# Kernel tuning notes

Measured on AMD Instinct MI355X. Metric: run time of the kernel, lower is better.

## Reference

```python
import jax, jax.numpy as jnp
import numpy as np

D_MODEL = 768
N_HEADS = 12
D_FF = 3072
B, T = 1, 4096
EPS = 1e-5


def _linear_params(key, d_in, d_out):
    kw, kb = jax.random.split(key)
    s = 1.0 / np.sqrt(d_in)
    W = jax.random.uniform(kw, (d_in, d_out), jnp.float32, -s, s)
    b = jax.random.uniform(kb, (d_out,), jnp.float32, -s, s)
    return W, b


def setup_inputs() -> dict:
    key = jax.random.key(0)
    keys = jax.random.split(key, 8)
    x = jax.random.normal(keys[0], (B, T, D_MODEL), jnp.float32)
    Wq, bq = _linear_params(keys[1], D_MODEL, D_MODEL)
    Wk, bk = _linear_params(keys[2], D_MODEL, D_MODEL)
    Wv, bv = _linear_params(keys[3], D_MODEL, D_MODEL)
    Wo, bo = _linear_params(keys[4], D_MODEL, D_MODEL)
    W1, b1 = _linear_params(keys[5], D_MODEL, D_FF)
    W2, b2 = _linear_params(keys[6], D_FF, D_MODEL)
    g1 = jnp.ones((D_MODEL,), jnp.float32)
    be1 = jnp.zeros((D_MODEL,), jnp.float32)
    g2 = jnp.ones((D_MODEL,), jnp.float32)
    be2 = jnp.zeros((D_MODEL,), jnp.float32)
    return {"x": x, "Wq": Wq, "bq": bq, "Wk": Wk, "bk": bk, "Wv": Wv, "bv": bv,
            "Wo": Wo, "bo": bo, "W1": W1, "b1": b1, "W2": W2, "b2": b2,
            "g1": g1, "be1": be1, "g2": g2, "be2": be2}


def _layer_norm(x, g, b):
    mu = jnp.mean(x, axis=-1, keepdims=True)
    var = jnp.var(x, axis=-1, keepdims=True)
    return (x - mu) * jax.lax.rsqrt(var + EPS) * g + b


def reference(x, Wq, bq, Wk, bk, Wv, bv, Wo, bo, W1, b1, W2, b2, g1, be1, g2, be2):
    b_, t_, d_ = x.shape
    dk = d_ // N_HEADS
    # QKV projections -> [B, H, T, dk]
    def split_heads(y):
        return y.reshape(b_, t_, N_HEADS, dk).transpose(0, 2, 1, 3)
    q = split_heads(x @ Wq + bq)
    k = split_heads(x @ Wk + bk)
    v = split_heads(x @ Wv + bv)
    # scores [B, H, T, T], causal mask, softmax
    scores = jnp.einsum('bhqd,bhkd->bhqk', q, k) / np.sqrt(dk).astype(np.float32)
    causal = jnp.tril(jnp.ones((t_, t_), dtype=bool))
    scores = jnp.where(causal, scores, -jnp.inf)
    attn = jax.nn.softmax(scores, axis=-1)
    out = jnp.einsum('bhqk,bhkd->bhqd', attn, v)
    out = out.transpose(0, 2, 1, 3).reshape(b_, t_, d_)
    attn_out = out @ Wo + bo
    # residual + LN1
    h = _layer_norm(x + attn_out, g1, be1)
    # FFN
    ff = jax.nn.relu(h @ W1 + b1) @ W2 + b2
    # residual + LN2
    return _layer_norm(h + ff, g2, be2)
```

## Files before the change

kernel.cpp:

```cpp
#include <hip/hip_runtime.h>
#include <math.h>

#define TSEQ 4096
#define DMODEL 768
#define NHEADS 12
#define DKH 64
#define DFF 3072
#define LOG2E 1.44269504f

typedef __attribute__((ext_vector_type(4))) float f32x4;
typedef __attribute__((ext_vector_type(8))) short s16x8;
typedef unsigned short u16;
typedef unsigned int u32;

__device__ __forceinline__ u16 f2bf(float x) {
    u32 u = __builtin_bit_cast(u32, x);
    u32 r = u + 0x7FFFu + ((u >> 16) & 1u);
    return (u16)(r >> 16);
}
__device__ __forceinline__ float bf2f(u16 h) {
    u32 u = ((u32)h) << 16;
    return __builtin_bit_cast(float, u);
}
__device__ __forceinline__ u32 cvtpk(float lo, float hi) {
    u32 r;
    asm("v_cvt_pk_bf16_f32 %0, %1, %2" : "=v"(r) : "v"(lo), "v"(hi));
    return r;
}

__device__ __forceinline__ void gll16(const void* g, void* lds) {
    __builtin_amdgcn_global_load_lds(
        (const __attribute__((address_space(1))) u32*)g,
        (__attribute__((address_space(3))) u32*)lds, 16, 0, 0);
}

__global__ __launch_bounds__(256) void tobf16(const float* __restrict__ in,
                                              u16* __restrict__ out, int n4)
{
    int idx = blockIdx.x * 256 + threadIdx.x;
    for (int i = idx; i < n4; i += 262144) {
        float4 v = *(const float4*)(in + (size_t)i * 4);
        *(ushort4*)(out + (size_t)i * 4) =
            make_ushort4(f2bf(v.x), f2bf(v.y), f2bf(v.z), f2bf(v.w));
    }
}

__global__ __launch_bounds__(256) void wtrans4(
    const float* __restrict__ Wq, const float* __restrict__ Wk,
    const float* __restrict__ Wv, const float* __restrict__ Wo,
    u16* __restrict__ Wqkvt, u16* __restrict__ Wot)
{
    __shared__ float t[32 * 33];
    const int z = blockIdx.z;
    const float* W = (z == 0) ? Wq : (z == 1) ? Wk : (z == 2) ? Wv : Wo;
    u16* out = (z < 3) ? Wqkvt : Wot;
    const int nofs = (z < 3) ? z * 768 : 0;
    const int K = 768, N = 768;
    const int tid = threadIdx.x;
    const int kt = blockIdx.y << 5, nt = blockIdx.x << 5;
    const int r = tid >> 3, c4 = tid & 7;
    float4 v = *(const float4*)(W + (size_t)(kt + r) * N + nt + (c4 << 2));
    t[r * 33 + (c4 << 2) + 0] = v.x;
    t[r * 33 + (c4 << 2) + 1] = v.y;
    t[r * 33 + (c4 << 2) + 2] = v.z;
    t[r * 33 + (c4 << 2) + 3] = v.w;
    __syncthreads();
    float a0 = t[((c4 << 2) + 0) * 33 + r];
    float a1 = t[((c4 << 2) + 1) * 33 + r];
    float a2 = t[((c4 << 2) + 2) * 33 + r];
    float a3 = t[((c4 << 2) + 3) * 33 + r];
    u16* o = out + (size_t)(nofs + nt + r) * K + kt + (c4 << 2);
    *(ushort4*)o = make_ushort4(f2bf(a0), f2bf(a1), f2bf(a2), f2bf(a3));
}

__global__ __launch_bounds__(256) void wtrans(const float* __restrict__ W,
                                              u16* __restrict__ out,
                                              int K, int N)
{
    __shared__ float t[32 * 33];
    const int tid = threadIdx.x;
    const int kt = blockIdx.y << 5, nt = blockIdx.x << 5;
    const int r = tid >> 3, c4 = tid & 7;
    float4 v = *(const float4*)(W + (size_t)(kt + r) * N + nt + (c4 << 2));
    t[r * 33 + (c4 << 2) + 0] = v.x;
    t[r * 33 + (c4 << 2) + 1] = v.y;
    t[r * 33 + (c4 << 2) + 2] = v.z;
    t[r * 33 + (c4 << 2) + 3] = v.w;
    __syncthreads();
    float a0 = t[((c4 << 2) + 0) * 33 + r];
    float a1 = t[((c4 << 2) + 1) * 33 + r];
    float a2 = t[((c4 << 2) + 2) * 33 + r];
    float a3 = t[((c4 << 2) + 3) * 33 + r];
    u16* o = out + (size_t)(nt + r) * K + kt + (c4 << 2);
    *(ushort4*)o = make_ushort4(f2bf(a0), f2bf(a1), f2bf(a2), f2bf(a3));
}

__global__ __launch_bounds__(256) void bias_cat_kernel(const float* bq, const float* bk,
                                                       const float* bv, float* o)
{
    int i = blockIdx.x * 256 + threadIdx.x;
    if (i < 768) o[i] = bq[i];
    else if (i < 1536) o[i] = bk[i - 768];
    else if (i < 2304) o[i] = bv[i - 1536];
}

template<int BM, int BN, int EPI>
__global__ __launch_bounds__(256) void gemm_bf(
    const u16* __restrict__ A, const u16* __restrict__ B,
    const float* __restrict__ bias, const float* __restrict__ R,
    float* __restrict__ Cf, u16* __restrict__ Cs,
    u16* __restrict__ Qb, u16* __restrict__ Kb, u16* __restrict__ VTb,
    int N, int KP)
{
    constexpr int FM = BM / 32, FN = BN / 32, NC = BN / 2, NCP = NC + 4;
    __shared__ u16 As[BM * 64];
    __shared__ u16 Bs[BN * 64];
    __shared__ float Ep[4 * 16 * NCP];

    const int tid = threadIdx.x;
    const int w = tid >> 6, lane = tid & 63;
    const int wr = w >> 1, wc = w & 1;
    const int li = lane & 15, g = lane >> 4;

    const int gX = gridDim.x;
    const int nwg = gridDim.x * gridDim.y;
    const int wid = blockIdx.y * gX + blockIdx.x;
    const int qc = nwg >> 3;
    const int nid = (wid & 7) * qc + (wid >> 3);
    const int m0 = (nid / gX) * BM, n0 = (nid % gX) * BN;

    f32x4 acc[FM][FN];
#pragma unroll
    for (int mi = 0; mi < FM; ++mi)
#pragma unroll
        for (int ni = 0; ni < FN; ++ni) acc[mi][ni] = (f32x4){0.f, 0.f, 0.f, 0.f};

    const int row8 = lane >> 3;
    const int cs = (lane & 7) ^ row8;
    const int l7 = li & 7;

    for (int k0 = 0; k0 < KP; k0 += 64) {
        __syncthreads();
#pragma unroll
        for (int i = 0; i < BM / 32; ++i) {
            int inst = w * (BM / 32) + i;
            const u16* gp = A + (size_t)(m0 + inst * 8 + row8) * KP + k0 + cs * 8;
            gll16(gp, &As[inst * 512]);
        }
#pragma unroll
        for (int i = 0; i < BN / 32; ++i) {
            int inst = w * (BN / 32) + i;
            const u16* gp = B + (size_t)(n0 + inst * 8 + row8) * KP + k0 + cs * 8;
            gll16(gp, &Bs[inst * 512]);
        }
        __syncthreads();
        s16x8 af[FM][2], bfr[FN][2];
#pragma unroll
        for (int mi = 0; mi < FM; ++mi) {
            int Ra = wr * (BM / 2) + mi * 16 + li;
#pragma unroll
            for (int dc = 0; dc < 2; ++dc)
                af[mi][dc] = *(const s16x8*)&As[Ra * 64 + ((dc * 4 + g) ^ l7) * 8];
        }
#pragma unroll
        for (int ni = 0; ni < FN; ++ni) {
            int Rb = wc * (BN / 2) + ni * 16 + li;
#pragma unroll
            for (int dc = 0; dc < 2; ++dc)
                bfr[ni][dc] = *(const s16x8*)&Bs[Rb * 64 + ((dc * 4 + g) ^ l7) * 8];
        }
        __builtin_amdgcn_s_setprio(1);
#pragma unroll
        for (int mi = 0; mi < FM; ++mi)
#pragma unroll
            for (int ni = 0; ni < FN; ++ni) {
                acc[mi][ni] = __builtin_amdgcn_mfma_f32_16x16x32_bf16(
                    af[mi][0], bfr[ni][0], acc[mi][ni], 0, 0, 0);
                acc[mi][ni] = __builtin_amdgcn_mfma_f32_16x16x32_bf16(
                    af[mi][1], bfr[ni][1], acc[mi][ni], 0, 0, 0);
            }
        __builtin_amdgcn_s_setprio(0);
    }
    __syncthreads();

    float* ep = Ep + w * 16 * NCP;
    const int colbase = n0 + wc * NC;
    const int rr = lane >> 2, ch = lane & 3;

#pragma unroll
    for (int mi = 0; mi < FM; ++mi) {
#pragma unroll
        for (int ni = 0; ni < FN; ++ni)
#pragma unroll
            for (int r = 0; r < 4; ++r)
                ep[(g * 4 + r) * NCP + ni * 16 + li] = acc[mi][ni][r];
        asm volatile("s_waitcnt lgkmcnt(0)" ::: "memory");

        const int grow0 = m0 + wr * (BM / 2) + mi * 16;
        const int grow = grow0 + rr;

        if constexpr (EPI == 1) {
#pragma unroll
            for (int q = 0; q < NC / 16; ++q) {
                int col = ch * (NC / 4) + q * 4;
                f32x4 v = *(f32x4*)&ep[rr * NCP + col];
                int gn = colbase + col;
                float4 bb = *(const float4*)(bias + gn);
                float4 rv = *(const float4*)(R + (size_t)grow * N + gn);
                float4 ov;
                ov.x = v[0] + bb.x + rv.x; ov.y = v[1] + bb.y + rv.y;
                ov.z = v[2] + bb.z + rv.z; ov.w = v[3] + bb.w + rv.w;
                *(float4*)(Cf + (size_t)grow * N + gn) = ov;
            }
        } else if constexpr (EPI == 2) {
#pragma unroll
            for (int q = 0; q < NC / 16; ++q) {
                int col = ch * (NC / 4) + q * 4;
                f32x4 v = *(f32x4*)&ep[rr * NCP + col];
                int gn = colbase + col;
                float4 bb = *(const float4*)(bias + gn);
                float x0 = fmaxf(v[0] + bb.x, 0.f), x1 = fmaxf(v[1] + bb.y, 0.f);
                float x2 = fmaxf(v[2] + bb.z, 0.f), x3 = fmaxf(v[3] + bb.w, 0.f);
                *(ushort4*)(Cs + (size_t)grow * N + gn) =
                    make_ushort4(f2bf(x0), f2bf(x1), f2bf(x2), f2bf(x3));
            }
        } else {
            const int seg = colbase / 768;
            const int hh = (colbase % 768) >> 6;
            if (seg < 2) {
                u16* dst = (seg == 0) ? Qb : Kb;
                const float sc2 = (seg == 0) ? 0.125f * LOG2E : 1.0f;
#pragma unroll
                for (int q = 0; q < NC / 16; ++q) {
                    int col = ch * (NC / 4) + q * 4;
                    f32x4 v = *(f32x4*)&ep[rr * NCP + col];
                    float4 bb = *(const float4*)(bias + colbase + col);
                    u16 h0 = f2bf((v[0] + bb.x) * sc2);
                    u16 h1 = f2bf((v[1] + bb.y) * sc2);
                    u16 h2 = f2bf((v[2] + bb.z) * sc2);
                    u16 h3 = f2bf((v[3] + bb.w) * sc2);
                    *(ushort4*)&dst[((size_t)(hh << 12) + grow) * 64 + col] =
                        make_ushort4(h0, h1, h2, h3);
                }
            } else {
                float bb = bias[colbase + lane];
                s16x8 pa, pb;
#pragma unroll
                for (int r2 = 0; r2 < 8; ++r2)
                    pa[r2] = (short)f2bf(ep[r2 * NCP + lane] + bb);
#pragma unroll
                for (int r2 = 0; r2 < 8; ++r2)
                    pb[r2] = (short)f2bf(ep[(8 + r2) * NCP + lane] + bb);
                u16* ov = VTb + ((size_t)(hh << 6) + lane) * TSEQ + grow0;
                *(s16x8*)(ov)     = pa;
                *(s16x8*)(ov + 8) = pb;
            }
        }
    }
}

__global__ __launch_bounds__(256) void attn64(
    const u16* __restrict__ Qb, const u16* __restrict__ Kb,
    const u16* __restrict__ VTb, u16* __restrict__ ctxb)
{
    __shared__ u16 Ks[2][4096];
    __shared__ u16 Vs[2][4096];
    __shared__ u16 Ps[4][1024];

    const int tid = threadIdx.x, w = tid >> 6, lane = tid & 63;
    const int g = lane >> 4, li = lane & 15, l7 = lane & 7;
    const int wid = blockIdx.x;
    const int nid = (wid & 7) * 48 + (wid >> 3);
    const int h = nid >> 5;
    const int p = nid & 31;

    const u16* Qh = Qb + ((size_t)h << 18);
    const u16* Kh = Kb + ((size_t)h << 18);
    const u16* Vh = VTb + ((size_t)h << 18);

    const int row8 = lane >> 3;
    const int cs = (lane & 7) ^ row8;

    for (int pass = 0; pass < 2; ++pass) {
        const int qbk = pass ? 63 - p : p;
        const int q0 = qbk << 6;
        const int nkb = qbk + 1;

        s16x8 qf[2];
#pragma unroll
        for (int dc = 0; dc < 2; ++dc)
            qf[dc] = *(const s16x8*)(Qh + (size_t)(q0 + w * 16 + li) * 64 + dc * 32 + g * 8);

        const u16* kbase = Kh + (size_t)(w * 16 + row8) * 64 + cs * 8;
        const u16* vbase = Vh + (size_t)(w * 16 + row8) * TSEQ + cs * 8;

        f32x4 o[4];
        float m_ = -1e30f, l_ = 0.f;
#pragma unroll
        for (int d16 = 0; d16 < 4; ++d16) o[d16] = (f32x4){0.f, 0.f, 0.f, 0.f};

#pragma unroll
        for (int i = 0; i < 2; ++i) {
            int inst = w * 2 + i;
            gll16(kbase + (size_t)i * 512, &Ks[0][inst * 512]);
            gll16(vbase + (size_t)i * 8 * TSEQ, &Vs[0][inst * 512]);
        }
        __syncthreads();

        for (int kb = 0; kb < nkb; ++kb) {
            const int cur = kb & 1;
            if (kb + 1 < nkb) {
                const int kn = kb + 1;
#pragma unroll
                for (int i = 0; i < 2; ++i) {
                    int inst = w * 2 + i;
                    gll16(kbase + (size_t)kn * 4096 + (size_t)i * 512, &Ks[cur ^ 1][inst * 512]);
                    gll16(vbase + (size_t)kn * 64 + (size_t)i * 8 * TSEQ, &Vs[cur ^ 1][inst * 512]);
                }
            }

            f32x4 s[4];
            __builtin_amdgcn_s_setprio(1);
#pragma unroll
            for (int c = 0; c < 4; ++c) {
                s[c] = (f32x4){0.f, 0.f, 0.f, 0.f};
                s16x8 a0 = *(const s16x8*)&Ks[cur][(c * 16 + li) * 64 + ((g) ^ l7) * 8];
                s16x8 a1 = *(const s16x8*)&Ks[cur][(c * 16 + li) * 64 + ((4 + g) ^ l7) * 8];
                s[c] = __builtin_amdgcn_mfma_f32_16x16x32_bf16(a0, qf[0], s[c], 0, 0, 0);
                s[c] = __builtin_amdgcn_mfma_f32_16x16x32_bf16(a1, qf[1], s[c], 0, 0, 0);
            }
            __builtin_amdgcn_s_setprio(0);

            if (kb == qbk) {
#pragma unroll
                for (int c = 0; c < 4; ++c)
#pragma unroll
                    for (int r = 0; r < 4; ++r) {
                        int kglob = (kb << 6) + c * 16 + g * 4 + r;
                        int qglob = q0 + w * 16 + li;
                        if (kglob > qglob) s[c][r] = -1e30f;
                    }
            }

            float v0 = fmaxf(fmaxf(s[0][0], s[0][1]), fmaxf(s[0][2], s[0][3]));
            float v1 = fmaxf(fmaxf(s[1][0], s[1][1]), fmaxf(s[1][2], s[1][3]));
            float v2 = fmaxf(fmaxf(s[2][0], s[2][1]), fmaxf(s[2][2], s[2][3]));
            float v3 = fmaxf(fmaxf(s[3][0], s[3][1]), fmaxf(s[3][2], s[3][3]));
            float pmp = fmaxf(fmaxf(v0, v1), fmaxf(v2, v3));

            if (!__all(pmp <= m_ + 8.f)) {
                float pm = fmaxf(pmp, __shfl_xor(pmp, 16, 64));
                pm = fmaxf(pm, __shfl_xor(pm, 32, 64));
                float mn = fmaxf(m_, pm);
                float sc2 = exp2f(m_ - mn);
                m_ = mn;
                l_ *= sc2;
#pragma unroll
                for (int r = 0; r < 4; ++r) {
                    float os = __shfl(sc2, g * 4 + r, 64);
#pragma unroll
                    for (int d16 = 0; d16 < 4; ++d16) o[d16][r] *= os;
                }
            }

#pragma unroll
            for (int c = 0; c < 4; ++c) {
                float e0 = exp2f(s[c][0] - m_);
                float e1 = exp2f(s[c][1] - m_);
                float e2 = exp2f(s[c][2] - m_);
                float e3 = exp2f(s[c][3] - m_);
                l_ += (e0 + e1) + (e2 + e3);
                u32 r0 = cvtpk(e0, e1);
                u32 r1 = cvtpk(e2, e3);
                *(uint2*)&Ps[w][li * 64 + ((c * 16 + 4 * g) ^ (l7 << 3))] =
                    make_uint2(r0, r1);
            }

            asm volatile("s_waitcnt lgkmcnt(0)" ::: "memory");
            __builtin_amdgcn_sched_barrier(0);

            __builtin_amdgcn_s_setprio(1);
#pragma unroll
            for (int ks = 0; ks < 2; ++ks) {
                int koff = ((ks * 4 + g) ^ l7) * 8;
                s16x8 pf = *(const s16x8*)&Ps[w][li * 64 + ((ks * 32 + g * 8) ^ (l7 << 3))];
#pragma unroll
                for (int d16 = 0; d16 < 4; ++d16) {
                    s16x8 vf = *(const s16x8*)&Vs[cur][(d16 * 16 + li) * 64 + koff];
                    o[d16] = __builtin_amdgcn_mfma_f32_16x16x32_bf16(pf, vf, o[d16], 0, 0, 0);
                }
            }
            __builtin_amdgcn_s_setprio(0);
            __syncthreads();
        }

        l_ += __shfl_xor(l_, 16, 64);
        l_ += __shfl_xor(l_, 32, 64);
        float il = 1.0f / l_;
#pragma unroll
        for (int r = 0; r < 4; ++r) {
            float iv = __shfl(il, g * 4 + r, 64);
            int qrow = q0 + w * 16 + g * 4 + r;
#pragma unroll
            for (int d16 = 0; d16 < 4; ++d16) {
                int col = (h << 6) + d16 * 16 + li;
                ctxb[(size_t)qrow * DMODEL + col] = f2bf(o[d16][r] * iv);
            }
        }
        __syncthreads();
    }
}

template<int BF>
__global__ __launch_bounds__(256) void ln_kernel(const float* __restrict__ in,
    const float* __restrict__ gw, const float* __restrict__ bw,
    float* __restrict__ outf, u16* __restrict__ outb)
{
    __shared__ float red[8];
    const int row = blockIdx.x, tid = threadIdx.x;
    const float* x = in + (size_t)row * DMODEL;
    float v0 = x[tid], v1 = x[tid + 256], v2 = x[tid + 512];
    float s = v0 + v1 + v2;
#pragma unroll
    for (int off = 32; off > 0; off >>= 1) s += __shfl_xor(s, off, 64);
    const int wv = tid >> 6, lane = tid & 63;
    if (lane == 0) red[wv] = s;
    __syncthreads();
    float mu = (red[0] + red[1] + red[2] + red[3]) * (1.0f / DMODEL);
    float d0 = v0 - mu, d1 = v1 - mu, d2 = v2 - mu;
    float s2 = d0 * d0 + d1 * d1 + d2 * d2;
#pragma unroll
    for (int off = 32; off > 0; off >>= 1) s2 += __shfl_xor(s2, off, 64);
    if (lane == 0) red[4 + wv] = s2;
    __syncthreads();
    float var = (red[4] + red[5] + red[6] + red[7]) * (1.0f / DMODEL);
    float rstd = rsqrtf(var + 1e-5f);
    float y0 = d0 * rstd * gw[tid] + bw[tid];
    float y1 = d1 * rstd * gw[tid + 256] + bw[tid + 256];
    float y2 = d2 * rstd * gw[tid + 512] + bw[tid + 512];
    float* yo = outf + (size_t)row * DMODEL;
    yo[tid] = y0; yo[tid + 256] = y1; yo[tid + 512] = y2;
    if constexpr (BF) {
        u16* o = outb + (size_t)row * DMODEL;
        o[tid] = f2bf(y0); o[tid + 256] = f2bf(y1); o[tid + 512] = f2bf(y2);
    }
}

extern "C" void kernel_launch(void* const* d_in, const int* in_sizes, int n_in,
                              void* d_out, int out_size, void* d_ws, size_t ws_size,
                              hipStream_t stream)
{
    const float* x  = (const float*)d_in[0];
    const float* Wq = (const float*)d_in[1];  const float* bq = (const float*)d_in[2];
    const float* Wk = (const float*)d_in[3];  const float* bk = (const float*)d_in[4];
    const float* Wv = (const float*)d_in[5];  const float* bv = (const float*)d_in[6];
    const float* Wo = (const float*)d_in[7];  const float* bo = (const float*)d_in[8];
    const float* W1 = (const float*)d_in[9];  const float* b1 = (const float*)d_in[10];
    const float* W2 = (const float*)d_in[11]; const float* b2 = (const float*)d_in[12];
    const float* g1 = (const float*)d_in[13]; const float* be1 = (const float*)d_in[14];
    const float* g2 = (const float*)d_in[15]; const float* be2 = (const float*)d_in[16];
    float* out = (float*)d_out;

    char* wsb = (char*)d_ws;
    u16*   xb    = (u16*)(wsb + 0);
    u16*   Wqkvt = (u16*)(wsb + 6291456);
    u16*   Wot   = (u16*)(wsb + 9830400);
    u16*   W1t   = (u16*)(wsb + 11010048);
    u16*   W2t   = (u16*)(wsb + 15728640);
    float* bcat  = (float*)(wsb + 20447232);
    u16*   Qb    = (u16*)(wsb + 20456448);
    u16*   Kb2   = (u16*)(wsb + 26747904);
    u16*   VTb   = (u16*)(wsb + 33039360);
    u16*   ctxb  = (u16*)(wsb + 39330816);
    float* s1    = (float*)(wsb + 45622272);
    float* h     = (float*)(wsb + 58205184);
    u16*   hb    = (u16*)(wsb + 70788096);
    u16*   ff1b  = (u16*)(wsb + 77079552);
    float* t2    = (float*)(wsb + 102245376);

    tobf16<<<1024, 256, 0, stream>>>(x, xb, 786432);
    wtrans4<<<dim3(24, 24, 4), 256, 0, stream>>>(Wq, Wk, Wv, Wo, Wqkvt, Wot);
    wtrans<<<dim3(96, 24), 256, 0, stream>>>(W1, W1t, 768, 3072);
    wtrans<<<dim3(24, 96), 256, 0, stream>>>(W2, W2t, 3072, 768);
    bias_cat_kernel<<<9, 256, 0, stream>>>(bq, bk, bv, bcat);

    gemm_bf<128, 128, 0><<<dim3(18, 32), 256, 0, stream>>>(
        xb, Wqkvt, bcat, nullptr, nullptr, nullptr, Qb, Kb2, VTb, 2304, 768);
    attn64<<<384, 256, 0, stream>>>(Qb, Kb2, VTb, ctxb);
    gemm_bf<64, 128, 1><<<dim3(6, 64), 256, 0, stream>>>(
        ctxb, Wot, bo, x, s1, nullptr, nullptr, nullptr, nullptr, 768, 768);
    ln_kernel<1><<<4096, 256, 0, stream>>>(s1, g1, be1, h, hb);
    gemm_bf<128, 128, 2><<<dim3(24, 32), 256, 0, stream>>>(
        hb, W1t, b1, nullptr, nullptr, ff1b, nullptr, nullptr, nullptr, 3072, 768);
    gemm_bf<64, 128, 1><<<dim3(6, 64), 256, 0, stream>>>(
        ff1b, W2t, b2, h, t2, nullptr, nullptr, nullptr, nullptr, 768, 3072);
    ln_kernel<0><<<4096, 256, 0, stream>>>(t2, g2, be2, out, nullptr);
}
```

Baseline: 372.7 us.

## Split attention KV range in two and merge partials in a combine kernel

Turns the causal attention kernel into a split-KV (flash-decoding style) variant. Each query block's key range is divided into two halves handled by separate workgroups, doubling the grid to 768 blocks. Each half writes unnormalized fp32 partial outputs plus row max and sum, and a new combine kernel rescales, merges and converts them to bf16. The aim is more parallelism and better load balance on the GPU, at the cost of extra fp32 partial traffic through global memory, one more kernel launch, and reuse of workspace regions that later kernels also use.

```diff
diff --git a/kernel.cpp b/kernel.cpp
--- a/kernel.cpp
+++ b/kernel.cpp
@@ -259,9 +259,10 @@
     }
 }
 
-__global__ __launch_bounds__(256) void attn64(
+__global__ __launch_bounds__(256) void attn64sp(
     const u16* __restrict__ Qb, const u16* __restrict__ Kb,
-    const u16* __restrict__ VTb, u16* __restrict__ ctxb)
+    const u16* __restrict__ VTb, float* __restrict__ Opart,
+    float* __restrict__ Mp, float* __restrict__ Lp)
 {
     __shared__ u16 Ks[2][4096];
     __shared__ u16 Vs[2][4096];
@@ -270,9 +271,11 @@
     const int tid = threadIdx.x, w = tid >> 6, lane = tid & 63;
     const int g = lane >> 4, li = lane & 15, l7 = lane & 7;
     const int wid = blockIdx.x;
-    const int nid = (wid & 7) * 48 + (wid >> 3);
-    const int h = nid >> 5;
-    const int p = nid & 31;
+    const int nid = (wid & 7) * 96 + (wid >> 3);
+    const int h = nid >> 6;
+    const int rest = nid & 63;
+    const int p = rest & 31;
+    const int split = rest >> 5;
 
     const u16* Qh = Qb + ((size_t)h << 18);
     const u16* Kh = Kb + ((size_t)h << 18);
@@ -284,7 +287,10 @@
     for (int pass = 0; pass < 2; ++pass) {
         const int qbk = pass ? 63 - p : p;
         const int q0 = qbk << 6;
-        const int nkb = qbk + 1;
+        const int nkf = qbk + 1;
+        const int half = (nkf + 1) >> 1;
+        const int kb0 = split ? half : 0;
+        const int kbe = split ? nkf : half;
 
         s16x8 qf[2];
 #pragma unroll
@@ -299,116 +305,146 @@
 #pragma unroll
         for (int d16 = 0; d16 < 4; ++d16) o[d16] = (f32x4){0.f, 0.f, 0.f, 0.f};
 
-#pragma unroll
-        for (int i = 0; i < 2; ++i) {
-            int inst = w * 2 + i;
-            gll16(kbase + (size_t)i * 512, &Ks[0][inst * 512]);
-            gll16(vbase + (size_t)i * 8 * TSEQ, &Vs[0][inst * 512]);
-        }
-        __syncthreads();
-
-        for (int kb = 0; kb < nkb; ++kb) {
-            const int cur = kb & 1;
-            if (kb + 1 < nkb) {
-                const int kn = kb + 1;
-#pragma unroll
-                for (int i = 0; i < 2; ++i) {
-                    int inst = w * 2 + i;
-                    gll16(kbase + (size_t)kn * 4096 + (size_t)i * 512, &Ks[cur ^ 1][inst * 512]);
-                    gll16(vbase + (size_t)kn * 64 + (size_t)i * 8 * TSEQ, &Vs[cur ^ 1][inst * 512]);
-                }
-            }
-
-            f32x4 s[4];
-            __builtin_amdgcn_s_setprio(1);
-#pragma unroll
-            for (int c = 0; c < 4; ++c) {
-                s[c] = (f32x4){0.f, 0.f, 0.f, 0.f};
-                s16x8 a0 = *(const s16x8*)&Ks[cur][(c * 16 + li) * 64 + ((g) ^ l7) * 8];
-                s16x8 a1 = *(const s16x8*)&Ks[cur][(c * 16 + li) * 64 + ((4 + g) ^ l7) * 8];
-                s[c] = __builtin_amdgcn_mfma_f32_16x16x32_bf16(a0, qf[0], s[c], 0, 0, 0);
-                s[c] = __builtin_amdgcn_mfma_f32_16x16x32_bf16(a1, qf[1], s[c], 0, 0, 0);
-            }
-            __builtin_amdgcn_s_setprio(0);
-
-            if (kb == qbk) {
-#pragma unroll
-                for (int c = 0; c < 4; ++c)
+        if (kb0 < kbe) {
+#pragma unroll
+            for (int i = 0; i < 2; ++i) {
+                int inst = w * 2 + i;
+                gll16(kbase + (size_t)kb0 * 4096 + (size_t)i * 512, &Ks[0][inst * 512]);
+                gll16(vbase + (size_t)kb0 * 64 + (size_t)i * 8 * TSEQ, &Vs[0][inst * 512]);
+            }
+            __syncthreads();
+
+            for (int kb = kb0; kb < kbe; ++kb) {
+                const int cur = (kb - kb0) & 1;
+                if (kb + 1 < kbe) {
+                    const int kn = kb + 1;
+#pragma unroll
+                    for (int i = 0; i < 2; ++i) {
+                        int inst = w * 2 + i;
+                        gll16(kbase + (size_t)kn * 4096 + (size_t)i * 512, &Ks[cur ^ 1][inst * 512]);
+                        gll16(vbase + (size_t)kn * 64 + (size_t)i * 8 * TSEQ, &Vs[cur ^ 1][inst * 512]);
+                    }
+                }
+
+                f32x4 s[4];
+                __builtin_amdgcn_s_setprio(1);
+#pragma unroll
+                for (int c = 0; c < 4; ++c) {
+                    s[c] = (f32x4){0.f, 0.f, 0.f, 0.f};
+                    s16x8 a0 = *(const s16x8*)&Ks[cur][(c * 16 + li) * 64 + ((g) ^ l7) * 8];
+                    s16x8 a1 = *(const s16x8*)&Ks[cur][(c * 16 + li) * 64 + ((4 + g) ^ l7) * 8];
+                    s[c] = __builtin_amdgcn_mfma_f32_16x16x32_bf16(a0, qf[0], s[c], 0, 0, 0);
+                    s[c] = __builtin_amdgcn_mfma_f32_16x16x32_bf16(a1, qf[1], s[c], 0, 0, 0);
+                }
+                __builtin_amdgcn_s_setprio(0);
+
+                if (kb == qbk) {
+#pragma unroll
+                    for (int c = 0; c < 4; ++c)
+#pragma unroll
+                        for (int r = 0; r < 4; ++r) {
+                            int kglob = (kb << 6) + c * 16 + g * 4 + r;
+                            int qglob = q0 + w * 16 + li;
+                            if (kglob > qglob) s[c][r] = -1e30f;
+                        }
+                }
+
+                float v0 = fmaxf(fmaxf(s[0][0], s[0][1]), fmaxf(s[0][2], s[0][3]));
+                float v1 = fmaxf(fmaxf(s[1][0], s[1][1]), fmaxf(s[1][2], s[1][3]));
+                float v2 = fmaxf(fmaxf(s[2][0], s[2][1]), fmaxf(s[2][2], s[2][3]));
+                float v3 = fmaxf(fmaxf(s[3][0], s[3][1]), fmaxf(s[3][2], s[3][3]));
+                float pmp = fmaxf(fmaxf(v0, v1), fmaxf(v2, v3));
+
+                if (!__all(pmp <= m_ + 8.f)) {
+                    float pm = fmaxf(pmp, __shfl_xor(pmp, 16, 64));
+                    pm = fmaxf(pm, __shfl_xor(pm, 32, 64));
+                    float mn = fmaxf(m_, pm);
+                    float sc2 = exp2f(m_ - mn);
+                    m_ = mn;
+                    l_ *= sc2;
 #pragma unroll
                     for (int r = 0; r < 4; ++r) {
-                        int kglob = (kb << 6) + c * 16 + g * 4 + r;
-                        int qglob = q0 + w * 16 + li;
-                        if (kglob > qglob) s[c][r] = -1e30f;
+                        float os = __shfl(sc2, g * 4 + r, 64);
+#pragma unroll
+                        for (int d16 = 0; d16 < 4; ++d16) o[d16][r] *= os;
                     }
-            }
-
-            float v0 = fmaxf(fmaxf(s[0][0], s[0][1]), fmaxf(s[0][2], s[0][3]));
-            float v1 = fmaxf(fmaxf(s[1][0], s[1][1]), fmaxf(s[1][2], s[1][3]));
-            float v2 = fmaxf(fmaxf(s[2][0], s[2][1]), fmaxf(s[2][2], s[2][3]));
-            float v3 = fmaxf(fmaxf(s[3][0], s[3][1]), fmaxf(s[3][2], s[3][3]));
-            float pmp = fmaxf(fmaxf(v0, v1), fmaxf(v2, v3));
-
-            if (!__all(pmp <= m_ + 8.f)) {
-                float pm = fmaxf(pmp, __shfl_xor(pmp, 16, 64));
-                pm = fmaxf(pm, __shfl_xor(pm, 32, 64));
-                float mn = fmaxf(m_, pm);
-                float sc2 = exp2f(m_ - mn);
-                m_ = mn;
-                l_ *= sc2;
-#pragma unroll
-                for (int r = 0; r < 4; ++r) {
-                    float os = __shfl(sc2, g * 4 + r, 64);
-#pragma unroll
-                    for (int d16 = 0; d16 < 4; ++d16) o[d16][r] *= os;
-                }
-            }
-
-#pragma unroll
-            for (int c = 0; c < 4; ++c) {
-                float e0 = exp2f(s[c][0] - m_);
-                float e1 = exp2f(s[c][1] - m_);
-                float e2 = exp2f(s[c][2] - m_);
-                float e3 = exp2f(s[c][3] - m_);
-                l_ += (e0 + e1) + (e2 + e3);
-                u32 r0 = cvtpk(e0, e1);
-                u32 r1 = cvtpk(e2, e3);
-                *(uint2*)&Ps[w][li * 64 + ((c * 16 + 4 * g) ^ (l7 << 3))] =
-                    make_uint2(r0, r1);
-            }
-
-            asm volatile("s_waitcnt lgkmcnt(0)" ::: "memory");
-            __builtin_amdgcn_sched_barrier(0);
-
-            __builtin_amdgcn_s_setprio(1);
-#pragma unroll
-            for (int ks = 0; ks < 2; ++ks) {
-                int koff = ((ks * 4 + g) ^ l7) * 8;
-                s16x8 pf = *(const s16x8*)&Ps[w][li * 64 + ((ks * 32 + g * 8) ^ (l7 << 3))];
-#pragma unroll
-                for (int d16 = 0; d16 < 4; ++d16) {
-                    s16x8 vf = *(const s16x8*)&Vs[cur][(d16 * 16 + li) * 64 + koff];
-                    o[d16] = __builtin_amdgcn_mfma_f32_16x16x32_bf16(pf, vf, o[d16], 0, 0, 0);
-                }
-            }
-            __builtin_amdgcn_s_setprio(0);
-            __syncthreads();
+                }
+
+#pragma unroll
+                for (int c = 0; c < 4; ++c) {
+                    float e0 = exp2f(s[c][0] - m_);
+                    float e1 = exp2f(s[c][1] - m_);
+                    float e2 = exp2f(s[c][2] - m_);
+                    float e3 = exp2f(s[c][3] - m_);
+                    l_ += (e0 + e1) + (e2 + e3);
+                    u32 r0 = cvtpk(e0, e1);
+                    u32 r1 = cvtpk(e2, e3);
+                    *(uint2*)&Ps[w][li * 64 + ((c * 16 + 4 * g) ^ (l7 << 3))] =
+                        make_uint2(r0, r1);
+                }
+
+                asm volatile("s_waitcnt lgkmcnt(0)" ::: "memory");
+                __builtin_amdgcn_sched_barrier(0);
+
+                __builtin_amdgcn_s_setprio(1);
+#pragma unroll
+                for (int ks = 0; ks < 2; ++ks) {
+                    int koff = ((ks * 4 + g) ^ l7) * 8;
+                    s16x8 pf = *(const s16x8*)&Ps[w][li * 64 + ((ks * 32 + g * 8) ^ (l7 << 3))];
+#pragma unroll
+                    for (int d16 = 0; d16 < 4; ++d16) {
+                        s16x8 vf = *(const s16x8*)&Vs[cur][(d16 * 16 + li) * 64 + koff];
+                        o[d16] = __builtin_amdgcn_mfma_f32_16x16x32_bf16(pf, vf, o[d16], 0, 0, 0);
+                    }
+                }
+                __builtin_amdgcn_s_setprio(0);
+                __syncthreads();
+            }
         }
 
         l_ += __shfl_xor(l_, 16, 64);
         l_ += __shfl_xor(l_, 32, 64);
-        float il = 1.0f / l_;
+        float* ob = Opart + (size_t)split * (TSEQ * DMODEL);
 #pragma unroll
         for (int r = 0; r < 4; ++r) {
-            float iv = __shfl(il, g * 4 + r, 64);
             int qrow = q0 + w * 16 + g * 4 + r;
 #pragma unroll
             for (int d16 = 0; d16 < 4; ++d16) {
                 int col = (h << 6) + d16 * 16 + li;
-                ctxb[(size_t)qrow * DMODEL + col] = f2bf(o[d16][r] * iv);
-            }
-        }
-        __syncthreads();
+                ob[(size_t)qrow * DMODEL + col] = o[d16][r];
+            }
+        }
+        if (g == 0) {
+            int qrow = q0 + w * 16 + li;
+            Mp[(size_t)(split * NHEADS + h) * TSEQ + qrow] = m_;
+            Lp[(size_t)(split * NHEADS + h) * TSEQ + qrow] = l_;
+        }
     }
+}
+
+__global__ __launch_bounds__(256) void attn_combine(
+    const float* __restrict__ Opart, const float* __restrict__ Mp,
+    const float* __restrict__ Lp, u16* __restrict__ ctxb)
+{
+    int idx = blockIdx.x * 256 + threadIdx.x;
+    int row = idx / 192;
+    int c4 = (idx - row * 192) << 2;
+    int h = c4 >> 6;
+    float m0 = Mp[(size_t)h * TSEQ + row];
+    float m1 = Mp[(size_t)(NHEADS + h) * TSEQ + row];
+    float l0 = Lp[(size_t)h * TSEQ + row];
+    float l1 = Lp[(size_t)(NHEADS + h) * TSEQ + row];
+    float M = fmaxf(m0, m1);
+    float w0 = exp2f(m0 - M), w1 = exp2f(m1 - M);
+    float iL = 1.0f / (w0 * l0 + w1 * l1);
+    float4 a = *(const float4*)(Opart + (size_t)row * DMODEL + c4);
+    float4 b = *(const float4*)(Opart + (size_t)(TSEQ * DMODEL) + (size_t)row * DMODEL + c4);
+    float x0 = (w0 * a.x + w1 * b.x) * iL;
+    float x1 = (w0 * a.y + w1 * b.y) * iL;
+    float x2 = (w0 * a.z + w1 * b.z) * iL;
+    float x3 = (w0 * a.w + w1 * b.w) * iL;
+    *(ushort4*)(ctxb + (size_t)row * DMODEL + c4) =
+        make_ushort4(f2bf(x0), f2bf(x1), f2bf(x2), f2bf(x3));
 }
 
 template<int BF>
@@ -477,6 +513,9 @@
     u16*   hb    = (u16*)(wsb + 70788096);
     u16*   ff1b  = (u16*)(wsb + 77079552);
     float* t2    = (float*)(wsb + 102245376);
+    float* Opart = (float*)(wsb + 45622272);
+    float* Mp    = (float*)(wsb + 70788096);
+    float* Lp    = (float*)(wsb + 71181312);
 
     tobf16<<<1024, 256, 0, stream>>>(x, xb, 786432);
     wtrans4<<<dim3(24, 24, 4), 256, 0, stream>>>(Wq, Wk, Wv, Wo, Wqkvt, Wot);
@@ -486,7 +525,8 @@
 
     gemm_bf<128, 128, 0><<<dim3(18, 32), 256, 0, stream>>>(
         xb, Wqkvt, bcat, nullptr, nullptr, nullptr, Qb, Kb2, VTb, 2304, 768);
-    attn64<<<384, 256, 0, stream>>>(Qb, Kb2, VTb, ctxb);
+    attn64sp<<<768, 256, 0, stream>>>(Qb, Kb2, VTb, Opart, Mp, Lp);
+    attn_combine<<<3072, 256, 0, stream>>>(Opart, Mp, Lp, ctxb);
     gemm_bf<64, 128, 1><<<dim3(6, 64), 256, 0, stream>>>(
         ctxb, Wot, bo, x, s1, nullptr, nullptr, nullptr, nullptr, 768, 768);
     ln_kernel<1><<<4096, 256, 0, stream>>>(s1, g1, be1, h, hb);
```

Measured after the change: 347.8 us. -6.7%, faster.
